# Performance work log

Hardware: AMD Instinct MI355X
Metric: run time of the kernel (lower is better)

Reference implementation:

```python
import jax, jax.numpy as jnp
import numpy as np
import math

D_MODEL = 768
N_HEADS = 12
D_HEAD = D_MODEL // N_HEADS
B, T = 2, 2048
EPS = 1e-5


def _layernorm(x, g, b):
    mu = jnp.mean(x, axis=-1, keepdims=True)
    var = jnp.var(x, axis=-1, keepdims=True)
    return (x - mu) * jax.lax.rsqrt(var + EPS) * g + b


def setup_inputs() -> dict:
    key = jax.random.key(0)
    ks = jax.random.split(key, 16)
    s = 0.02
    inp = {
        "x": jax.random.normal(ks[0], (B, T, D_MODEL), jnp.float32),
        "q_pos": jax.random.normal(ks[1], (B, N_HEADS, T, D_HEAD), jnp.float32),
        "k_pos": jax.random.normal(ks[2], (B, N_HEADS, T, D_HEAD), jnp.float32),
        "causal_mask": jnp.triu(jnp.ones((T, T), dtype=bool), k=1),
        "Wq": jax.random.normal(ks[3], (D_MODEL, D_MODEL), jnp.float32) * s,
        "bq": jnp.zeros((D_MODEL,), jnp.float32),
        "Wk": jax.random.normal(ks[4], (D_MODEL, D_MODEL), jnp.float32) * s,
        "bk": jnp.zeros((D_MODEL,), jnp.float32),
        "Wv": jax.random.normal(ks[5], (D_MODEL, D_MODEL), jnp.float32) * s,
        "bv": jnp.zeros((D_MODEL,), jnp.float32),
        "Wo": jax.random.normal(ks[6], (D_MODEL, D_MODEL), jnp.float32) * s,
        "bo": jnp.zeros((D_MODEL,), jnp.float32),
        "ln1_g": jnp.ones((D_MODEL,), jnp.float32),
        "ln1_b": jnp.zeros((D_MODEL,), jnp.float32),
        "ln2_g": jnp.ones((D_MODEL,), jnp.float32),
        "ln2_b": jnp.zeros((D_MODEL,), jnp.float32),
        "W1": jax.random.normal(ks[7], (D_MODEL, 4 * D_MODEL), jnp.float32) * s,
        "b1": jnp.zeros((4 * D_MODEL,), jnp.float32),
        "W2": jax.random.normal(ks[8], (4 * D_MODEL, D_MODEL), jnp.float32) * s,
        "b2": jnp.zeros((D_MODEL,), jnp.float32),
    }
    return inp


def reference(x, q_pos, k_pos, causal_mask, Wq, bq, Wk, bk, Wv, bv, Wo, bo,
              ln1_g, ln1_b, ln2_g, ln2_b, W1, b1, W2, b2):
    h = _layernorm(x, ln1_g, ln1_b)  # [B,T,D]
    # project and split heads -> [B,H,T,d]
    def heads(y):
        return y.reshape(B, T, N_HEADS, D_HEAD).transpose(0, 2, 1, 3)
    Qc = heads(h @ Wq + bq)
    Kc = heads(h @ Wk + bk)
    V = heads(h @ Wv + bv)
    scale = math.sqrt(D_HEAD)
    A_X = jnp.einsum('bhqd,bhkd->bhqk', Qc, Kc) / scale
    A_P = jnp.einsum('bhqd,bhkd->bhqk', q_pos, k_pos) / scale
    scores = A_X * A_P  # Hadamard combination of content + positional scores
    scores = jnp.where(causal_mask[None, None, :, :], -jnp.inf, scores)
    attn = jax.nn.softmax(scores, axis=-1)
    out = jnp.einsum('bhqk,bhkd->bhqd', attn, V)  # [B,H,T,d]
    out = out.transpose(0, 2, 1, 3).reshape(B, T, D_MODEL)
    out = out @ Wo + bo
    x = x + out
    h2 = _layernorm(x, ln2_g, ln2_b)
    ffn = jax.nn.gelu(h2 @ W1 + b1, approximate=False) @ W2 + b2
    return x + ffn
```

## Files before the change

### kernel.cpp

```cpp
#include <hip/hip_runtime.h>
#include <hip/hip_bf16.h>
#include <math.h>

#define D_MODEL 768
#define N_HEADS 12
#define D_HEAD  64
#define BATCH   2
#define SEQ     2048
#define ROWS    (BATCH*SEQ)
#define D_FFN   (4*D_MODEL)

typedef short bf16x8 __attribute__((ext_vector_type(8)));
typedef float f32x4  __attribute__((ext_vector_type(4)));

__device__ __forceinline__ short f2bf(float f) {
    __hip_bfloat16 h = __float2bfloat16(f);
    return *reinterpret_cast<short*>(&h);
}

template<int CTRL>
__device__ __forceinline__ float dpp_f(float x) {
    int v = __builtin_amdgcn_update_dpp(0, __float_as_int(x), CTRL, 0xF, 0xF, true);
    return __int_as_float(v);
}
__device__ __forceinline__ float dpp_max16(float x) {
    x = fmaxf(x, dpp_f<0xB1>(x));
    x = fmaxf(x, dpp_f<0x4E>(x));
    x = fmaxf(x, dpp_f<0x141>(x));
    x = fmaxf(x, dpp_f<0x140>(x));
    return x;
}
__device__ __forceinline__ float dpp_sum16(float x) {
    x += dpp_f<0xB1>(x);
    x += dpp_f<0x4E>(x);
    x += dpp_f<0x141>(x);
    x += dpp_f<0x140>(x);
    return x;
}

__global__ __launch_bounds__(256)
void prep_kernel(const float* __restrict__ Wq, const float* __restrict__ Wk,
                 const float* __restrict__ Wv, const float* __restrict__ Wo,
                 const float* __restrict__ W1, const float* __restrict__ W2,
                 const float* __restrict__ q_pos, const float* __restrict__ k_pos,
                 short* __restrict__ WTq, short* __restrict__ WTk,
                 short* __restrict__ WTv, short* __restrict__ WTo,
                 short* __restrict__ WT1, short* __restrict__ WT2,
                 short* __restrict__ qp_bf, short* __restrict__ kp_bf) {
    int id = blockIdx.x;
    if (id >= 6912) {
        int cid = id - 6912;
        bool isq = (cid < 1536);
        int c = isq ? cid : cid - 1536;
        const float* src = isq ? q_pos : k_pos;
        short* dst = isq ? qp_bf : kp_bf;
        int i = (c * 256 + threadIdx.x) * 8;
        float4 a = *reinterpret_cast<const float4*>(src + i);
        float4 b = *reinterpret_cast<const float4*>(src + i + 4);
        bf16x8 r;
        r[0]=f2bf(a.x); r[1]=f2bf(a.y); r[2]=f2bf(a.z); r[3]=f2bf(a.w);
        r[4]=f2bf(b.x); r[5]=f2bf(b.y); r[6]=f2bf(b.z); r[7]=f2bf(b.w);
        *reinterpret_cast<bf16x8*>(dst + i) = r;
        return;
    }
    const float* W; short* WT; int K, N, t;
    if (id < 576)        { W = Wq; WT = WTq; K = 768;  N = 768;  t = id; }
    else if (id < 1152)  { W = Wk; WT = WTk; K = 768;  N = 768;  t = id - 576; }
    else if (id < 1728)  { W = Wv; WT = WTv; K = 768;  N = 768;  t = id - 1152; }
    else if (id < 2304)  { W = Wo; WT = WTo; K = 768;  N = 768;  t = id - 1728; }
    else if (id < 4608)  { W = W1; WT = WT1; K = 768;  N = 3072; t = id - 2304; }
    else                 { W = W2; WT = WT2; K = 3072; N = 768;  t = id - 4608; }
    int nb = N >> 5;
    int n0 = (t % nb) * 32, k0 = (t / nb) * 32;
    __shared__ float tile[32][33];
    int tx = threadIdx.x & 31, ty = threadIdx.x >> 5;
    #pragma unroll
    for (int i = 0; i < 4; ++i)
        tile[ty + 8*i][tx] = W[(size_t)(k0 + ty + 8*i) * N + n0 + tx];
    __syncthreads();
    #pragma unroll
    for (int i = 0; i < 4; ++i)
        WT[(size_t)(n0 + ty + 8*i) * K + k0 + tx] = f2bf(tile[tx][ty + 8*i]);
}

__global__ __launch_bounds__(256)
void transpose_v_kernel(const short* __restrict__ Vm, short* __restrict__ Vt) {
    __shared__ short tile[64][72];
    int kt = blockIdx.x;
    int bh = blockIdx.y;
    int b = bh / N_HEADS, h = bh % N_HEADS;
    int tid = threadIdx.x;
    int row = tid >> 2, c16 = (tid & 3) * 16;
    const short* src = Vm + ((size_t)(b * SEQ) + kt * 64 + row) * D_MODEL + h * 64 + c16;
    *reinterpret_cast<bf16x8*>(&tile[row][c16])     = *reinterpret_cast<const bf16x8*>(src);
    *reinterpret_cast<bf16x8*>(&tile[row][c16 + 8]) = *reinterpret_cast<const bf16x8*>(src + 8);
    __syncthreads();
    int d = tid >> 2, k16 = (tid & 3) * 16;
    short o[16];
    #pragma unroll
    for (int j = 0; j < 16; ++j) o[j] = tile[k16 + j][d];
    short* dst = Vt + ((size_t)bh * 64 + d) * SEQ + kt * 64 + k16;
    *reinterpret_cast<bf16x8*>(dst)     = *reinterpret_cast<bf16x8*>(&o[0]);
    *reinterpret_cast<bf16x8*>(dst + 8) = *reinterpret_cast<bf16x8*>(&o[8]);
}

__global__ __launch_bounds__(256)
void ln_kernel(const float* __restrict__ x, const float* __restrict__ g,
               const float* __restrict__ beta, short* __restrict__ out) {
    int row = blockIdx.x;
    const float* xr = x + (size_t)row * D_MODEL;
    int t = threadIdx.x;
    float v0 = xr[t], v1 = xr[t + 256], v2 = xr[t + 512];
    float s  = v0 + v1 + v2;
    float s2 = v0*v0 + v1*v1 + v2*v2;
    __shared__ float rs[4], rs2[4];
    #pragma unroll
    for (int off = 32; off; off >>= 1) {
        s  += __shfl_down(s, off);
        s2 += __shfl_down(s2, off);
    }
    int wv = t >> 6, ln = t & 63;
    if (ln == 0) { rs[wv] = s; rs2[wv] = s2; }
    __syncthreads();
    float S  = rs[0] + rs[1] + rs[2] + rs[3];
    float S2 = rs2[0] + rs2[1] + rs2[2] + rs2[3];
    float mu  = S * (1.0f / D_MODEL);
    float var = S2 * (1.0f / D_MODEL) - mu * mu;
    float inv = rsqrtf(var + 1e-5f);
    short* orow = out + (size_t)row * D_MODEL;
    orow[t]       = f2bf((v0 - mu) * inv * g[t]       + beta[t]);
    orow[t + 256] = f2bf((v1 - mu) * inv * g[t + 256] + beta[t + 256]);
    orow[t + 512] = f2bf((v2 - mu) * inv * g[t + 512] + beta[t + 512]);
}

template<int ACT, bool RES, bool OUTBF>
__device__ __forceinline__
void gemm_body(const short* __restrict__ A, const short* __restrict__ WT,
               const float* __restrict__ bias, const float* __restrict__ res,
               void* __restrict__ Cout, int M, int N, int K) {
    __shared__ short As[128 * 32];
    __shared__ short Bs[128 * 32];
    const int tid = threadIdx.x;
    const int w = tid >> 6, lane = tid & 63;
    const int lr = lane & 15, lg = lane >> 4;
    const int wm = w >> 1, wn = w & 1;
    const int bm = blockIdx.y * 128, bn = blockIdx.x * 128;

    f32x4 acc[4][4] = {};

    const int srow = w * 32 + (lane >> 2);
    const int scol = (lane & 3) * 8;
    const short* Ag = A  + (size_t)(bm + srow) * K + scol;
    const short* Bg = WT + (size_t)(bn + srow) * K + scol;

    for (int k0 = 0; k0 < K; k0 += 32) {
        __syncthreads();
        #pragma unroll
        for (int r = 0; r < 2; ++r) {
            __builtin_amdgcn_global_load_lds(
                (const __attribute__((address_space(1))) void*)(Ag + (size_t)r * 16 * K + k0),
                (__attribute__((address_space(3))) void*)(As + w * 1024 + r * 512),
                16, 0, 0);
            __builtin_amdgcn_global_load_lds(
                (const __attribute__((address_space(1))) void*)(Bg + (size_t)r * 16 * K + k0),
                (__attribute__((address_space(3))) void*)(Bs + w * 1024 + r * 512),
                16, 0, 0);
        }
        __syncthreads();
        bf16x8 af[4], bfr[4];
        #pragma unroll
        for (int mi = 0; mi < 4; ++mi)
            af[mi] = *reinterpret_cast<const bf16x8*>(As + (wm*64 + mi*16 + lr) * 32 + lg*8);
        #pragma unroll
        for (int nj = 0; nj < 4; ++nj)
            bfr[nj] = *reinterpret_cast<const bf16x8*>(Bs + (wn*64 + nj*16 + lr) * 32 + lg*8);
        #pragma unroll
        for (int mi = 0; mi < 4; ++mi)
            #pragma unroll
            for (int nj = 0; nj < 4; ++nj)
                acc[mi][nj] = __builtin_amdgcn_mfma_f32_16x16x32_bf16(af[mi], bfr[nj], acc[mi][nj], 0, 0, 0);
    }

    float bias_v[4];
    #pragma unroll
    for (int nj = 0; nj < 4; ++nj) bias_v[nj] = bias[bn + wn*64 + nj*16 + lr];

    #pragma unroll
    for (int mi = 0; mi < 4; ++mi) {
        #pragma unroll
        for (int j = 0; j < 4; ++j) {
            size_t m = bm + wm*64 + mi*16 + lg*4 + j;
            #pragma unroll
            for (int nj = 0; nj < 4; ++nj) {
                size_t n = bn + wn*64 + nj*16 + lr;
                float v = acc[mi][nj][j] + bias_v[nj];
                if (RES) v += res[m * N + n];
                if (ACT == 1) v = 0.5f * v * (1.0f + erff(v * 0.70710678118f));
                if (OUTBF) ((short*)Cout)[m * N + n] = f2bf(v);
                else       ((float*)Cout)[m * N + n] = v;
            }
        }
    }
}

template<int ACT, bool RES, bool OUTBF>
__global__ __launch_bounds__(256)
void gemm_mfma_kernel(const short* __restrict__ A, const short* __restrict__ WT,
                      const float* __restrict__ bias, const float* __restrict__ res,
                      void* __restrict__ Cout, int M, int N, int K) {
    gemm_body<ACT, RES, OUTBF>(A, WT, bias, res, Cout, M, N, K);
}

__global__ __launch_bounds__(256)
void gemm_qkv_kernel(const short* __restrict__ A,
                     const short* __restrict__ WTq, const short* __restrict__ WTk,
                     const short* __restrict__ WTv,
                     const float* __restrict__ bq, const float* __restrict__ bk,
                     const float* __restrict__ bv,
                     short* __restrict__ Qm, short* __restrict__ Km, short* __restrict__ Vm) {
    const short* WT; const float* bias; short* C;
    if (blockIdx.z == 0)      { WT = WTq; bias = bq; C = Qm; }
    else if (blockIdx.z == 1) { WT = WTk; bias = bk; C = Km; }
    else                      { WT = WTv; bias = bv; C = Vm; }
    gemm_body<0, false, true>(A, WT, bias, nullptr, C, ROWS, D_MODEL, D_MODEL);
}

__global__ __launch_bounds__(256)
void attn_mfma_kernel(const short* __restrict__ Q, const short* __restrict__ K,
                      const short* __restrict__ Vt, const short* __restrict__ qp,
                      const short* __restrict__ kp, short* __restrict__ ao) {
    __shared__ short Ks[2][4096];
    __shared__ short kps[2][4096];
    __shared__ short Vts[2][4096];
    __shared__ short Plds[4][16][76];

    int lin = blockIdx.x;
    int wid = (lin & 7) * 96 + (lin >> 3);
    int bh = wid >> 5;
    int qb = 31 - (wid & 31);
    int b = bh / N_HEADS, h = bh % N_HEADS;
    int tid = threadIdx.x, w = tid >> 6, lane = tid & 63;
    int lr = lane & 15, lg = lane >> 4;

    const short* Kh  = K  + (size_t)(b * SEQ) * D_MODEL + h * 64;
    const short* kph = kp + (size_t)bh * SEQ * 64;
    const short* Vth = Vt + (size_t)bh * 64 * SEQ;

    const int s_sub  = lane >> 3;
    const int s_colb = ((lane & 7) ^ s_sub) << 4;

    auto stage = [&](int kt, int buf) {
        #pragma unroll
        for (int j = 0; j < 2; ++j) {
            int row = (w * 2 + j) * 8 + s_sub;
            int ldsoff = (w * 2 + j) * 1024;
            __builtin_amdgcn_global_load_lds(
                (const __attribute__((address_space(1))) void*)
                    ((const char*)(Kh + (size_t)(kt * 64 + row) * D_MODEL) + s_colb),
                (__attribute__((address_space(3))) void*)((char*)&Ks[buf][0] + ldsoff), 16, 0, 0);
            __builtin_amdgcn_global_load_lds(
                (const __attribute__((address_space(1))) void*)
                    ((const char*)(kph + (size_t)(kt * 64 + row) * 64) + s_colb),
                (__attribute__((address_space(3))) void*)((char*)&kps[buf][0] + ldsoff), 16, 0, 0);
            __builtin_amdgcn_global_load_lds(
                (const __attribute__((address_space(1))) void*)
                    ((const char*)(Vth + (size_t)row * SEQ + kt * 64) + s_colb),
                (__attribute__((address_space(3))) void*)((char*)&Vts[buf][0] + ldsoff), 16, 0, 0);
        }
    };
    auto ldr = [&](const short* base, int row, int halfb) -> bf16x8 {
        int off = row * 128 + ((halfb + lg * 16) ^ ((row & 7) << 4));
        return *reinterpret_cast<const bf16x8*>((const char*)base + off);
    };

    int qbase = qb * 64 + w * 16;
    const short* Qrow  = Q  + ((size_t)(b * SEQ) + qbase + lr) * D_MODEL + h * 64;
    const short* qprow = qp + ((size_t)bh * SEQ + qbase + lr) * 64;
    bf16x8 qf0  = *reinterpret_cast<const bf16x8*>(Qrow + lg * 8);
    bf16x8 qf1  = *reinterpret_cast<const bf16x8*>(Qrow + 32 + lg * 8);
    bf16x8 qpf0 = *reinterpret_cast<const bf16x8*>(qprow + lg * 8);
    bf16x8 qpf1 = *reinterpret_cast<const bf16x8*>(qprow + 32 + lg * 8);

    f32x4 o_acc[4] = {};
    float m_run[4], l_run[4];
    #pragma unroll
    for (int r = 0; r < 4; ++r) { m_run[r] = -1e30f; l_run[r] = 0.f; }

    int nkt = qb + 1;
    stage(0, 0);
    __syncthreads();
    int cur = 0;

    for (int kt = 0; kt < nkt; ++kt) {
        if (kt + 1 < nkt) stage(kt + 1, cur ^ 1);

        const short* Kb  = &Ks[cur][0];
        const short* kpb = &kps[cur][0];
        const short* Vb  = &Vts[cur][0];
        f32x4 sx[4] = {}, sp[4] = {};
        __builtin_amdgcn_s_setprio(1);
        #pragma unroll
        for (int sub = 0; sub < 4; ++sub) {
            int row = sub * 16 + lr;
            bf16x8 kf0 = ldr(Kb, row, 0),  kf1 = ldr(Kb, row, 64);
            bf16x8 kq0 = ldr(kpb, row, 0), kq1 = ldr(kpb, row, 64);
            sx[sub] = __builtin_amdgcn_mfma_f32_16x16x32_bf16(qf0,  kf0, sx[sub], 0, 0, 0);
            sx[sub] = __builtin_amdgcn_mfma_f32_16x16x32_bf16(qf1,  kf1, sx[sub], 0, 0, 0);
            sp[sub] = __builtin_amdgcn_mfma_f32_16x16x32_bf16(qpf0, kq0, sp[sub], 0, 0, 0);
            sp[sub] = __builtin_amdgcn_mfma_f32_16x16x32_bf16(qpf1, kq1, sp[sub], 0, 0, 0);
        }
        __builtin_amdgcn_s_setprio(0);

        float sc[4][4];
        float pmax[4];
        bool diag = (kt == qb);
        #pragma unroll
        for (int r = 0; r < 4; ++r) {
            int row = qbase + lg * 4 + r;
            float mx = -1e30f;
            #pragma unroll
            for (int sub = 0; sub < 4; ++sub) {
                float v = sx[sub][r] * sp[sub][r] * (1.0f / 64.0f);
                if (diag) {
                    int col = kt * 64 + sub * 16 + lr;
                    if (col > row) v = -1e30f;
                }
                sc[sub][r] = v;
                mx = fmaxf(mx, v);
            }
            pmax[r] = dpp_max16(mx);
        }

        #pragma unroll
        for (int r = 0; r < 4; ++r) {
            float m_new = fmaxf(m_run[r], pmax[r]);
            float scale = __expf(m_run[r] - m_new);
            m_run[r] = m_new;
            float s = 0.f;
            #pragma unroll
            for (int sub = 0; sub < 4; ++sub) {
                float p = __expf(sc[sub][r] - m_new);
                sc[sub][r] = p;
                s += p;
            }
            l_run[r] = l_run[r] * scale + dpp_sum16(s);
            #pragma unroll
            for (int ds = 0; ds < 4; ++ds) o_acc[ds][r] *= scale;
        }

        #pragma unroll
        for (int sub = 0; sub < 4; ++sub)
            #pragma unroll
            for (int r = 0; r < 4; ++r)
                Plds[w][lg * 4 + r][sub * 16 + lr] = f2bf(sc[sub][r]);

        bf16x8 pa0 = *reinterpret_cast<bf16x8*>(&Plds[w][lr][lg * 8]);
        bf16x8 pa1 = *reinterpret_cast<bf16x8*>(&Plds[w][lr][32 + lg * 8]);

        __builtin_amdgcn_s_setprio(1);
        #pragma unroll
        for (int ds = 0; ds < 4; ++ds) {
            int row = ds * 16 + lr;
            bf16x8 vb0 = ldr(Vb, row, 0), vb1 = ldr(Vb, row, 64);
            o_acc[ds] = __builtin_amdgcn_mfma_f32_16x16x32_bf16(pa0, vb0, o_acc[ds], 0, 0, 0);
            o_acc[ds] = __builtin_amdgcn_mfma_f32_16x16x32_bf16(pa1, vb1, o_acc[ds], 0, 0, 0);
        }
        __builtin_amdgcn_s_setprio(0);

        __syncthreads();
        cur ^= 1;
    }

    #pragma unroll
    for (int ds = 0; ds < 4; ++ds)
        #pragma unroll
        for (int r = 0; r < 4; ++r) {
            int row = qbase + lg * 4 + r;
            float val = o_acc[ds][r] / l_run[r];
            ao[((size_t)(b * SEQ) + row) * D_MODEL + h * 64 + ds * 16 + lr] = f2bf(val);
        }
}

extern "C" void kernel_launch(void* const* d_in, const int* in_sizes, int n_in,
                              void* d_out, int out_size, void* d_ws, size_t ws_size,
                              hipStream_t stream) {
    const float* x     = (const float*)d_in[0];
    const float* q_pos = (const float*)d_in[1];
    const float* k_pos = (const float*)d_in[2];
    const float* Wq = (const float*)d_in[4];
    const float* bq = (const float*)d_in[5];
    const float* Wk = (const float*)d_in[6];
    const float* bk = (const float*)d_in[7];
    const float* Wv = (const float*)d_in[8];
    const float* bv = (const float*)d_in[9];
    const float* Wo = (const float*)d_in[10];
    const float* bo = (const float*)d_in[11];
    const float* ln1_g = (const float*)d_in[12];
    const float* ln1_b = (const float*)d_in[13];
    const float* ln2_g = (const float*)d_in[14];
    const float* ln2_b = (const float*)d_in[15];
    const float* W1 = (const float*)d_in[16];
    const float* b1 = (const float*)d_in[17];
    const float* W2 = (const float*)d_in[18];
    const float* b2 = (const float*)d_in[19];
    float* out = (float*)d_out;

    char* p = (char*)d_ws;
    auto alloc = [&](size_t bytes) { char* q = p; p += (bytes + 255) & ~(size_t)255; return q; };
    const size_t SA = (size_t)ROWS * D_MODEL;
    const size_t SP = (size_t)BATCH * N_HEADS * SEQ * 64;

    short* h_bf  = (short*)alloc(SA * 2);
    short* Qm    = (short*)alloc(SA * 2);
    short* Km    = (short*)alloc(SA * 2);
    short* Vm    = (short*)alloc(SA * 2);
    short* Vt    = (short*)alloc(SP * 2);
    short* ao    = (short*)alloc(SA * 2);
    short* qp_bf = (short*)alloc(SP * 2);
    short* kp_bf = (short*)alloc(SP * 2);
    short* mid   = (short*)alloc((size_t)ROWS * D_FFN * 2);
    float* x2    = (float*)alloc(SA * 4);
    short* WTq   = (short*)alloc((size_t)D_MODEL * D_MODEL * 2);
    short* WTk   = (short*)alloc((size_t)D_MODEL * D_MODEL * 2);
    short* WTv   = (short*)alloc((size_t)D_MODEL * D_MODEL * 2);
    short* WTo   = (short*)alloc((size_t)D_MODEL * D_MODEL * 2);
    short* WT1   = (short*)alloc((size_t)D_MODEL * D_FFN * 2);
    short* WT2   = (short*)alloc((size_t)D_MODEL * D_FFN * 2);

    prep_kernel<<<9984, 256, 0, stream>>>(Wq, Wk, Wv, Wo, W1, W2, q_pos, k_pos,
                                          WTq, WTk, WTv, WTo, WT1, WT2, qp_bf, kp_bf);

    ln_kernel<<<ROWS, 256, 0, stream>>>(x, ln1_g, ln1_b, h_bf);
    gemm_qkv_kernel<<<dim3(D_MODEL/128, ROWS/128, 3), 256, 0, stream>>>(
        h_bf, WTq, WTk, WTv, bq, bk, bv, Qm, Km, Vm);
    transpose_v_kernel<<<dim3(SEQ/64, BATCH*N_HEADS), 256, 0, stream>>>(Vm, Vt);
    attn_mfma_kernel<<<768, 256, 0, stream>>>(Qm, Km, Vt, qp_bf, kp_bf, ao);
    gemm_mfma_kernel<0, true, false><<<dim3(D_MODEL/128, ROWS/128), 256, 0, stream>>>(
        ao, WTo, bo, x, x2, ROWS, D_MODEL, D_MODEL);
    ln_kernel<<<ROWS, 256, 0, stream>>>(x2, ln2_g, ln2_b, h_bf);
    gemm_mfma_kernel<1, false, true><<<dim3(D_FFN/128, ROWS/128), 256, 0, stream>>>(
        h_bf, WT1, b1, nullptr, mid, ROWS, D_FFN, D_MODEL);
    gemm_mfma_kernel<0, true, false><<<dim3(D_MODEL/128, ROWS/128), 256, 0, stream>>>(
        mid, WT2, b2, x2, out, ROWS, D_MODEL, D_FFN);
}
```

Measured before the change: 258.9 us.

## Split-K the W2 GEMM and skip online-softmax rescale below threshold

Result: faster. 230.2 us (-11.1%).

```diff
diff --git a/kernel.cpp b/kernel.cpp
--- a/kernel.cpp
+++ b/kernel.cpp
@@ -137,7 +137,7 @@
 __device__ __forceinline__
 void gemm_body(const short* __restrict__ A, const short* __restrict__ WT,
                const float* __restrict__ bias, const float* __restrict__ res,
-               void* __restrict__ Cout, int M, int N, int K) {
+               void* __restrict__ Cout, int M, int N, int Kloop, int Kstride) {
     __shared__ short As[128 * 32];
     __shared__ short Bs[128 * 32];
     const int tid = threadIdx.x;
@@ -150,19 +150,19 @@
 
     const int srow = w * 32 + (lane >> 2);
     const int scol = (lane & 3) * 8;
-    const short* Ag = A  + (size_t)(bm + srow) * K + scol;
-    const short* Bg = WT + (size_t)(bn + srow) * K + scol;
-
-    for (int k0 = 0; k0 < K; k0 += 32) {
+    const short* Ag = A  + (size_t)(bm + srow) * Kstride + scol;
+    const short* Bg = WT + (size_t)(bn + srow) * Kstride + scol;
+
+    for (int k0 = 0; k0 < Kloop; k0 += 32) {
         __syncthreads();
         #pragma unroll
         for (int r = 0; r < 2; ++r) {
             __builtin_amdgcn_global_load_lds(
-                (const __attribute__((address_space(1))) void*)(Ag + (size_t)r * 16 * K + k0),
+                (const __attribute__((address_space(1))) void*)(Ag + (size_t)r * 16 * Kstride + k0),
                 (__attribute__((address_space(3))) void*)(As + w * 1024 + r * 512),
                 16, 0, 0);
             __builtin_amdgcn_global_load_lds(
-                (const __attribute__((address_space(1))) void*)(Bg + (size_t)r * 16 * K + k0),
+                (const __attribute__((address_space(1))) void*)(Bg + (size_t)r * 16 * Kstride + k0),
                 (__attribute__((address_space(3))) void*)(Bs + w * 1024 + r * 512),
                 16, 0, 0);
         }
@@ -181,9 +181,11 @@
                 acc[mi][nj] = __builtin_amdgcn_mfma_f32_16x16x32_bf16(af[mi], bfr[nj], acc[mi][nj], 0, 0, 0);
     }
 
-    float bias_v[4];
-    #pragma unroll
-    for (int nj = 0; nj < 4; ++nj) bias_v[nj] = bias[bn + wn*64 + nj*16 + lr];
+    float bias_v[4] = {0.f, 0.f, 0.f, 0.f};
+    if constexpr (ACT != 2) {
+        #pragma unroll
+        for (int nj = 0; nj < 4; ++nj) bias_v[nj] = bias[bn + wn*64 + nj*16 + lr];
+    }
 
     #pragma unroll
     for (int mi = 0; mi < 4; ++mi) {
@@ -208,7 +210,7 @@
 void gemm_mfma_kernel(const short* __restrict__ A, const short* __restrict__ WT,
                       const float* __restrict__ bias, const float* __restrict__ res,
                       void* __restrict__ Cout, int M, int N, int K) {
-    gemm_body<ACT, RES, OUTBF>(A, WT, bias, res, Cout, M, N, K);
+    gemm_body<ACT, RES, OUTBF>(A, WT, bias, res, Cout, M, N, K, K);
 }
 
 __global__ __launch_bounds__(256)
@@ -222,7 +224,33 @@
     if (blockIdx.z == 0)      { WT = WTq; bias = bq; C = Qm; }
     else if (blockIdx.z == 1) { WT = WTk; bias = bk; C = Km; }
     else                      { WT = WTv; bias = bv; C = Vm; }
-    gemm_body<0, false, true>(A, WT, bias, nullptr, C, ROWS, D_MODEL, D_MODEL);
+    gemm_body<0, false, true>(A, WT, bias, nullptr, C, ROWS, D_MODEL, D_MODEL, D_MODEL);
+}
+
+__global__ __launch_bounds__(256)
+void gemm_w2_kernel(const short* __restrict__ mid, const short* __restrict__ WT2,
+                    float* __restrict__ P0, float* __restrict__ P1) {
+    int z = blockIdx.z;
+    gemm_body<2, false, false>(mid + z * 1536, WT2 + z * 1536, nullptr, nullptr,
+                               z ? P1 : P0, ROWS, D_MODEL, 1536, D_FFN);
+}
+
+__global__ __launch_bounds__(256)
+void w2_epi_kernel(const float* __restrict__ P0, const float* __restrict__ P1,
+                   const float* __restrict__ b2, const float* __restrict__ x2,
+                   float* __restrict__ out) {
+    size_t i = ((size_t)blockIdx.x * 256 + threadIdx.x) * 4;
+    int n = (int)(i % D_MODEL);
+    float4 p0 = *reinterpret_cast<const float4*>(P0 + i);
+    float4 p1 = *reinterpret_cast<const float4*>(P1 + i);
+    float4 xr = *reinterpret_cast<const float4*>(x2 + i);
+    float4 bb = *reinterpret_cast<const float4*>(b2 + n);
+    float4 o;
+    o.x = p0.x + p1.x + xr.x + bb.x;
+    o.y = p0.y + p1.y + xr.y + bb.y;
+    o.z = p0.z + p1.z + xr.z + bb.z;
+    o.w = p0.w + p1.w + xr.w + bb.w;
+    *reinterpret_cast<float4*>(out + i) = o;
 }
 
 __global__ __launch_bounds__(256)
@@ -331,21 +359,30 @@
             pmax[r] = dpp_max16(mx);
         }
 
+        bool need = false;
+        #pragma unroll
+        for (int r = 0; r < 4; ++r) need = need || (pmax[r] > m_run[r] + 8.f);
+        if (__any(need)) {
+            #pragma unroll
+            for (int r = 0; r < 4; ++r) {
+                float m_new = fmaxf(m_run[r], pmax[r]);
+                float scale = __expf(m_run[r] - m_new);
+                m_run[r] = m_new;
+                l_run[r] *= scale;
+                #pragma unroll
+                for (int ds = 0; ds < 4; ++ds) o_acc[ds][r] *= scale;
+            }
+        }
         #pragma unroll
         for (int r = 0; r < 4; ++r) {
-            float m_new = fmaxf(m_run[r], pmax[r]);
-            float scale = __expf(m_run[r] - m_new);
-            m_run[r] = m_new;
             float s = 0.f;
             #pragma unroll
             for (int sub = 0; sub < 4; ++sub) {
-                float p = __expf(sc[sub][r] - m_new);
+                float p = __expf(sc[sub][r] - m_run[r]);
                 sc[sub][r] = p;
                 s += p;
             }
-            l_run[r] = l_run[r] * scale + dpp_sum16(s);
-            #pragma unroll
-            for (int ds = 0; ds < 4; ++ds) o_acc[ds][r] *= scale;
+            l_run[r] += dpp_sum16(s);
         }
 
         #pragma unroll
@@ -420,6 +457,8 @@
     short* kp_bf = (short*)alloc(SP * 2);
     short* mid   = (short*)alloc((size_t)ROWS * D_FFN * 2);
     float* x2    = (float*)alloc(SA * 4);
+    float* P0    = (float*)alloc(SA * 4);
+    float* P1    = (float*)alloc(SA * 4);
     short* WTq   = (short*)alloc((size_t)D_MODEL * D_MODEL * 2);
     short* WTk   = (short*)alloc((size_t)D_MODEL * D_MODEL * 2);
     short* WTv   = (short*)alloc((size_t)D_MODEL * D_MODEL * 2);
@@ -440,6 +479,6 @@
     ln_kernel<<<ROWS, 256, 0, stream>>>(x2, ln2_g, ln2_b, h_bf);
     gemm_mfma_kernel<1, false, true><<<dim3(D_FFN/128, ROWS/128), 256, 0, stream>>>(
         h_bf, WT1, b1, nullptr, mid, ROWS, D_FFN, D_MODEL);
-    gemm_mfma_kernel<0, true, false><<<dim3(D_MODEL/128, ROWS/128), 256, 0, stream>>>(
-        mid, WT2, b2, x2, out, ROWS, D_MODEL, D_FFN);
-}
+    gemm_w2_kernel<<<dim3(D_MODEL/128, ROWS/128, 2), 256, 0, stream>>>(mid, WT2, P0, P1);
+    w2_epi_kernel<<<(int)(SA/1024), 256, 0, stream>>>(P0, P1, b2, x2, out);
+}
```
